# Performance work log

Hardware: AMD Instinct MI355X
Metric: run time of the kernel (lower is better)

## Reference

```python
import jax, jax.numpy as jnp
import numpy as np

NEG = -1.0e30  # safe stand-in for -inf (avoids nan in gradients)
EPS = 1e-7     # keras.backend.epsilon()


def _ctc_loss(true_labels, true_lengths, y_pred, input_lengths):
    """CTC negative log-likelihood, matching keras.backend.ctc_batch_cost.

    true_labels:   [B, L] int labels (blank = V-1 excluded)
    true_lengths:  [B, 1] label lengths
    y_pred:        [B, T, V] softmax probabilities
    input_lengths: [B, 1] number of valid time frames
    returns:       [B, 1] loss
    """
    B, T, V = y_pred.shape
    L = true_labels.shape[1]
    S = 2 * L + 1
    blank = V - 1

    logp = jnp.log(y_pred + EPS)                                   # [B,T,V]

    # Extended label sequence: blank, l1, blank, l2, ..., blank
    ext = jnp.full((B, S), blank, dtype=true_labels.dtype)
    ext = ext.at[:, 1::2].set(true_labels)                          # [B,S]
    ext_m2 = jnp.concatenate(
        [jnp.full((B, 2), blank, dtype=ext.dtype), ext[:, :-2]], axis=1)
    s_idx = jnp.arange(S)
    can_skip = (s_idx >= 2)[None, :] & (ext != blank) & (ext != ext_m2)  # [B,S]

    # Per-extended-position log-probs at every time step: [B,T,S]
    lp_ext = jax.vmap(lambda lp_b, e_b: lp_b[:, e_b])(logp, ext)

    def step(alpha, inp):
        t, lp_t = inp                                               # lp_t [B,S]
        a1 = jnp.concatenate([jnp.full((B, 1), NEG), alpha[:, :-1]], axis=1)
        a2 = jnp.concatenate([jnp.full((B, 2), NEG), alpha[:, :-2]], axis=1)
        m = jnp.logaddexp(alpha, a1)
        m = jnp.where(can_skip, jnp.logaddexp(m, a2), m)
        new = m + lp_t
        # freeze alpha for sequences past their input length
        new = jnp.where(t < input_lengths, new, alpha)              # [B,1] bcast
        return new, None

    # alpha_{-1}: probability 1 at a virtual start before position 0
    alpha0 = jnp.full((B, S), NEG).at[:, 0].set(0.0)
    alpha, _ = jax.lax.scan(
        step, alpha0, (jnp.arange(T), jnp.transpose(lp_ext, (1, 0, 2))))

    lab = true_lengths[:, 0]
    b_idx = jnp.arange(B)
    a_last = alpha[b_idx, 2 * lab]          # ends at final blank
    a_prev = alpha[b_idx, 2 * lab - 1]      # ends at final label
    return -jnp.logaddexp(a_last, a_prev)[:, None]                  # [B,1]


def setup_inputs() -> dict:
    key = jax.random.key(0)
    k1, k2, k3 = jax.random.split(key, 3)
    B, T, V, L = 128, 1024, 512, 128
    logits = jax.random.normal(k1, (B, T, V), dtype=jnp.float32)
    predicted_labels = jax.nn.softmax(logits, axis=-1)              # probabilities
    true_labels = jax.random.randint(k2, (B, L), 0, V - 1)          # exclude blank
    true_lengths = jax.random.randint(k3, (B, 1), 16, L + 1)
    predicted_lengths = jnp.full((B, 1), T, dtype=jnp.int32)
    return {
        "true_labels": true_labels,
        "true_lengths": true_lengths,
        "predicted_labels": predicted_labels,
        "predicted_lengths": predicted_lengths,
    }


def reference(true_labels, true_lengths, predicted_labels, predicted_lengths):
    # CTCLayer.call returns predicted_labels and registers the loss via
    # add_loss; the computation of interest is the CTC loss itself.
    return _ctc_loss(true_labels, true_lengths, predicted_labels, predicted_lengths)
```

## Files before the change

### kernel.cpp

```cpp
#include <hip/hip_runtime.h>

constexpr int Tc = 1024;
constexpr int Vc = 512;
constexpr int Lc = 128;
constexpr int Sc = 2 * Lc + 1;
constexpr int BLANK = Vc - 1;
constexpr float NEGF = -1e30f;
constexpr float EPSF = 1e-7f;
constexpr int PF = 16;

__device__ __forceinline__ float lae2(float x, float y) {
    float m = fmaxf(x, y);
    return m + __logf(__expf(x - m) + __expf(y - m));
}
__device__ __forceinline__ float lae3(float x, float y, float z) {
    float m = fmaxf(fmaxf(x, y), z);
    return m + __logf(__expf(x - m) + __expf(y - m) + __expf(z - m));
}

__launch_bounds__(64, 1)
__global__ void ctc_fwd_wave(const int* __restrict__ labels,
                             const int* __restrict__ label_len,
                             const float* __restrict__ probs,
                             const int* __restrict__ input_len,
                             float* __restrict__ out)
{
    const int b    = blockIdx.x;
    const int lane = threadIdx.x;

    __shared__ float sa[Sc];

    const int lbase = b * Lc;
    const int l0  = labels[lbase + 2 * lane];
    const int l1  = labels[lbase + 2 * lane + 1];
    const int lm1 = (lane > 0) ? labels[lbase + 2 * lane - 1] : 0;
    const bool cs1 = (lane > 0) && (l0 != lm1);
    const bool cs3 = (l1 != l0);
    const int len = input_len[b];

    const float* __restrict__ base = probs + (size_t)b * Tc * Vc;
    const float* __restrict__ pB = base + BLANK;
    const float* __restrict__ p1 = base + l0;
    const float* __restrict__ p2 = base + l1;

    float rb[PF], r1[PF], r2[PF];
#pragma unroll
    for (int j = 0; j < PF; ++j) {
        const size_t o = (size_t)j * Vc;
        rb[j] = pB[o]; r1[j] = p1[o]; r2[j] = p2[o];
    }

    float a0 = (lane == 0) ? 0.0f : NEGF;
    float a1 = NEGF;
    float a2 = NEGF;
    float a3 = NEGF;
    float a4 = NEGF;

    auto step = [&](int t, int j, bool refill) {
        const float lpb = __logf(rb[j] + EPSF);
        const float lp1 = __logf(r1[j] + EPSF);
        const float lp2 = __logf(r2[j] + EPSF);
        if (refill) {
            const size_t o = (size_t)(t + PF) * Vc;
            rb[j] = pB[o]; r1[j] = p1[o]; r2[j] = p2[o];
        }
        float up3 = __shfl_up(a3, 1);
        if (lane == 0) up3 = NEGF;

        float n0 = lae2(a0, up3) + lpb;
        float n1 = lae3(a1, a0, cs1 ? up3 : NEGF) + lp1;
        float n2 = lae2(a2, a1) + lpb;
        float n3 = lae3(a3, a2, cs3 ? a1 : NEGF) + lp2;
        float n4 = lae2(a4, a3) + lpb;

        const bool live = (t < len);
        a0 = live ? n0 : a0;
        a1 = live ? n1 : a1;
        a2 = live ? n2 : a2;
        a3 = live ? n3 : a3;
        a4 = live ? n4 : a4;
    };

    for (int t0 = 0; t0 < Tc - PF; t0 += PF) {
#pragma unroll
        for (int j = 0; j < PF; ++j) step(t0 + j, j, true);
    }
#pragma unroll
    for (int j = 0; j < PF; ++j) step(Tc - PF + j, j, false);

    sa[4 * lane + 0] = a0;
    sa[4 * lane + 1] = a1;
    sa[4 * lane + 2] = a2;
    sa[4 * lane + 3] = a3;
    if (lane == 63) sa[256] = a4;
    __syncthreads();
    if (lane == 0) {
        const int lab = label_len[b];
        const float x = sa[2 * lab];
        const float y = sa[2 * lab - 1];
        out[b] = -lae2(x, y);
    }
}

extern "C" void kernel_launch(void* const* d_in, const int* in_sizes, int n_in,
                              void* d_out, int out_size, void* d_ws, size_t ws_size,
                              hipStream_t stream) {
    const int*   labels    = (const int*)d_in[0];
    const int*   label_len = (const int*)d_in[1];
    const float* probs     = (const float*)d_in[2];
    const int*   input_len = (const int*)d_in[3];
    float*       out       = (float*)d_out;

    const int B = in_sizes[1];
    ctc_fwd_wave<<<B, 64, 0, stream>>>(labels, label_len, probs, input_len, out);
}
```

Measured before the change: 739.5 us.

## Warp-specialize CTC: producer waves gather log-probs into double-buffered LDS chunks

Moves the CTC forward kernel from a single wave per sequence to a 512-thread block. Seven producer waves gather the needed label and blank probabilities for 128-timestep chunks, take their logs, and write them into a double-buffered shared-memory tile. One consumer wave runs the alpha recursion from LDS and reorders work so the shuffle of n3 overlaps the other updates. This is meant to hide global gather latency and take the log work off the serial recursion, at the cost of a block-wide barrier per chunk and more LDS.

```diff
diff --git a/kernel.cpp b/kernel.cpp
--- a/kernel.cpp
+++ b/kernel.cpp
@@ -7,7 +7,9 @@
 constexpr int BLANK = Vc - 1;
 constexpr float NEGF = -1e30f;
 constexpr float EPSF = 1e-7f;
-constexpr int PF = 16;
+constexpr int CHUNK = 128;
+constexpr int NCH = Tc / CHUNK;
+constexpr int CCOLS = 132;
 
 __device__ __forceinline__ float lae2(float x, float y) {
     float m = fmaxf(x, y);
@@ -18,84 +20,104 @@
     return m + __logf(__expf(x - m) + __expf(y - m) + __expf(z - m));
 }
 
-__launch_bounds__(64, 1)
-__global__ void ctc_fwd_wave(const int* __restrict__ labels,
-                             const int* __restrict__ label_len,
-                             const float* __restrict__ probs,
-                             const int* __restrict__ input_len,
-                             float* __restrict__ out)
+__launch_bounds__(512, 1)
+__global__ void ctc_fwd_pc(const int* __restrict__ labels,
+                           const int* __restrict__ label_len,
+                           const float* __restrict__ probs,
+                           const int* __restrict__ input_len,
+                           float* __restrict__ out)
 {
     const int b    = blockIdx.x;
-    const int lane = threadIdx.x;
+    const int tid  = threadIdx.x;
+    const int lane = tid & 63;
+    const int wv   = tid >> 6;
 
+    __shared__ __align__(16) float cbuf[2][CHUNK][CCOLS];
     __shared__ float sa[Sc];
+    __shared__ int   slab[Lc];
 
-    const int lbase = b * Lc;
-    const int l0  = labels[lbase + 2 * lane];
-    const int l1  = labels[lbase + 2 * lane + 1];
-    const int lm1 = (lane > 0) ? labels[lbase + 2 * lane - 1] : 0;
+    if (tid < Lc) slab[tid] = labels[b * Lc + tid];
+    __syncthreads();
+
+    const float* __restrict__ pb = probs + (size_t)b * Tc * Vc;
+
+    const int pc0 = slab[lane];
+    const int pc1 = slab[lane + 64];
+    auto fill = [&](int c) {
+        const int t0 = c * CHUNK;
+        float (* __restrict__ dst)[CCOLS] = cbuf[c & 1];
+#pragma unroll 2
+        for (int r = wv - 1; r < CHUNK; r += 7) {
+            const float* __restrict__ prow = pb + (size_t)(t0 + r) * Vc;
+            const float v0 = prow[pc0];
+            const float v1 = prow[pc1];
+            const float vb = (lane == 0) ? prow[BLANK] : 0.0f;
+            dst[r][lane]      = __logf(v0 + EPSF);
+            dst[r][lane + 64] = __logf(v1 + EPSF);
+            if (lane == 0) dst[r][128] = __logf(vb + EPSF);
+        }
+    };
+
+    const int l0  = slab[2 * lane];
+    const int l1  = slab[2 * lane + 1];
+    const int lm1 = (lane > 0) ? slab[2 * lane - 1] : 0;
     const bool cs1 = (lane > 0) && (l0 != lm1);
     const bool cs3 = (l1 != l0);
     const int len = input_len[b];
+    const int lab = label_len[b];
 
-    const float* __restrict__ base = probs + (size_t)b * Tc * Vc;
-    const float* __restrict__ pB = base + BLANK;
-    const float* __restrict__ p1 = base + l0;
-    const float* __restrict__ p2 = base + l1;
+    float a0 = (lane == 0) ? 0.0f : NEGF;
+    float a1 = NEGF, a2 = NEGF, a3 = NEGF, a4 = NEGF;
+    float u3 = NEGF;
 
-    float rb[PF], r1[PF], r2[PF];
-#pragma unroll
-    for (int j = 0; j < PF; ++j) {
-        const size_t o = (size_t)j * Vc;
-        rb[j] = pB[o]; r1[j] = p1[o]; r2[j] = p2[o];
+    if (wv != 0) fill(0);
+    __syncthreads();
+
+    for (int c = 0; c < NCH; ++c) {
+        if (wv != 0) {
+            if (c + 1 < NCH) fill(c + 1);
+        } else {
+            const float (* __restrict__ cb)[CCOLS] = cbuf[c & 1];
+            float2 pv = *(const float2*)&cb[0][2 * lane];
+            float  bv = cb[0][128];
+            for (int r = 0; r < CHUNK; ++r) {
+                float2 nv = pv; float nb = bv;
+                if (r + 1 < CHUNK) {
+                    nv = *(const float2*)&cb[r + 1][2 * lane];
+                    nb = cb[r + 1][128];
+                }
+                const int t = c * CHUNK + r;
+                const float lpb = bv;
+                const float lp1 = pv.x;
+                const float lp2 = pv.y;
+                const float n3 = lae3(a3, a2, cs3 ? a1 : NEGF) + lp2;
+                const float u3n = __shfl_up(n3, 1);
+                const float n0 = lae2(a0, u3) + lpb;
+                const float n1 = lae3(a1, a0, cs1 ? u3 : NEGF) + lp1;
+                const float n2 = lae2(a2, a1) + lpb;
+                const float n4 = lae2(a4, a3) + lpb;
+                const bool live = (t < len);
+                a0 = live ? n0 : a0;
+                a1 = live ? n1 : a1;
+                a2 = live ? n2 : a2;
+                a3 = live ? n3 : a3;
+                a4 = live ? n4 : a4;
+                u3 = live ? ((lane == 0) ? NEGF : u3n) : u3;
+                pv = nv; bv = nb;
+            }
+        }
+        __syncthreads();
     }
 
-    float a0 = (lane == 0) ? 0.0f : NEGF;
-    float a1 = NEGF;
-    float a2 = NEGF;
-    float a3 = NEGF;
-    float a4 = NEGF;
-
-    auto step = [&](int t, int j, bool refill) {
-        const float lpb = __logf(rb[j] + EPSF);
-        const float lp1 = __logf(r1[j] + EPSF);
-        const float lp2 = __logf(r2[j] + EPSF);
-        if (refill) {
-            const size_t o = (size_t)(t + PF) * Vc;
-            rb[j] = pB[o]; r1[j] = p1[o]; r2[j] = p2[o];
-        }
-        float up3 = __shfl_up(a3, 1);
-        if (lane == 0) up3 = NEGF;
-
-        float n0 = lae2(a0, up3) + lpb;
-        float n1 = lae3(a1, a0, cs1 ? up3 : NEGF) + lp1;
-        float n2 = lae2(a2, a1) + lpb;
-        float n3 = lae3(a3, a2, cs3 ? a1 : NEGF) + lp2;
-        float n4 = lae2(a4, a3) + lpb;
-
-        const bool live = (t < len);
-        a0 = live ? n0 : a0;
-        a1 = live ? n1 : a1;
-        a2 = live ? n2 : a2;
-        a3 = live ? n3 : a3;
-        a4 = live ? n4 : a4;
-    };
-
-    for (int t0 = 0; t0 < Tc - PF; t0 += PF) {
-#pragma unroll
-        for (int j = 0; j < PF; ++j) step(t0 + j, j, true);
+    if (wv == 0) {
+        sa[4 * lane + 0] = a0;
+        sa[4 * lane + 1] = a1;
+        sa[4 * lane + 2] = a2;
+        sa[4 * lane + 3] = a3;
+        if (lane == 63) sa[256] = a4;
     }
-#pragma unroll
-    for (int j = 0; j < PF; ++j) step(Tc - PF + j, j, false);
-
-    sa[4 * lane + 0] = a0;
-    sa[4 * lane + 1] = a1;
-    sa[4 * lane + 2] = a2;
-    sa[4 * lane + 3] = a3;
-    if (lane == 63) sa[256] = a4;
     __syncthreads();
-    if (lane == 0) {
-        const int lab = label_len[b];
+    if (tid == 0) {
         const float x = sa[2 * lab];
         const float y = sa[2 * lab - 1];
         out[b] = -lae2(x, y);
@@ -112,5 +134,5 @@
     float*       out       = (float*)d_out;
 
     const int B = in_sizes[1];
-    ctc_fwd_wave<<<B, 64, 0, stream>>>(labels, label_len, probs, input_len, out);
+    ctc_fwd_pc<<<B, 512, 0, stream>>>(labels, label_len, probs, input_len, out);
 }
```

Result: faster. 601.0 us (-18.7%).
